# Optimization experiments

Measured on AMD Instinct MI355X. Metric: run time of the kernel, lower is better.

The kernel has to match this reference:

```python
import jax, jax.numpy as jnp
import numpy as np

LN_EPS = 1e-6

def _ln_proj(x, ln_scale, ln_bias, kernel, bias):
    # LayerNorm over last dim, then GEMM projection. Dropout is identity
    # (deterministic / eval mode, training=False default).
    mu = jnp.mean(x, axis=-1, keepdims=True)
    var = jnp.mean(jnp.square(x - mu), axis=-1, keepdims=True)
    xn = (x - mu) * jax.lax.rsqrt(var + LN_EPS) * ln_scale + ln_bias
    return jnp.einsum('bsh,hp->bsp', xn, kernel) + bias


def setup_inputs() -> dict:
    key = jax.random.key(0)
    ks = jax.random.split(key, 4)
    B, S, H, P = 2, 4096, 4096, 1024
    return {
        'vision_features': jax.random.normal(ks[0], (B, S, H), dtype=jnp.float32),
        'text_features': jax.random.normal(ks[1], (B, S, H), dtype=jnp.float32),
        'v_ln_scale': jnp.ones((H,), jnp.float32),
        'v_ln_bias': jnp.zeros((H,), jnp.float32),
        'v_kernel': jax.random.normal(ks[2], (H, P), dtype=jnp.float32) / np.sqrt(H).astype(np.float32),
        'v_bias': jnp.zeros((P,), jnp.float32),
        't_ln_scale': jnp.ones((H,), jnp.float32),
        't_ln_bias': jnp.zeros((H,), jnp.float32),
        't_kernel': jax.random.normal(ks[3], (H, P), dtype=jnp.float32) / np.sqrt(H).astype(np.float32),
        't_bias': jnp.zeros((P,), jnp.float32),
    }


def reference(vision_features, text_features, v_ln_scale, v_ln_bias, v_kernel, v_bias,
              t_ln_scale, t_ln_bias, t_kernel, t_bias):
    vision_projected = _ln_proj(vision_features, v_ln_scale, v_ln_bias, v_kernel, v_bias)
    text_projected = _ln_proj(text_features, t_ln_scale, t_ln_bias, t_kernel, t_bias)
    return (vision_projected, text_projected)
```

## Files before the change

kernel.cpp:

```cpp
#include <hip/hip_runtime.h>
#include <hip/hip_bf16.h>
#include <stdint.h>

#define LN_EPS 1e-6f

typedef __bf16 bf16x8 __attribute__((ext_vector_type(8)));
typedef float f32x4 __attribute__((ext_vector_type(4)));

__device__ __forceinline__ unsigned short f2bf(float f) {
    uint32_t u = __float_as_uint(f);
    uint32_t r = (u + 0x7fffu + ((u >> 16) & 1u)) >> 16;
    return (unsigned short)r;
}

__device__ __forceinline__ void async_copy16(const void* g, void* l) {
    const __attribute__((address_space(1))) uint32_t* gp =
        (const __attribute__((address_space(1))) uint32_t*)(uintptr_t)g;
    __attribute__((address_space(3))) uint32_t* lp =
        (__attribute__((address_space(3))) uint32_t*)(uint32_t)(uintptr_t)l;
    __builtin_amdgcn_global_load_lds(gp, lp, 16, 0, 0);
}

__global__ __launch_bounds__(256) void ln_bf16_kernel(
    const float* __restrict__ x0, const float* __restrict__ x1,
    const float* __restrict__ s0, const float* __restrict__ b0,
    const float* __restrict__ s1, const float* __restrict__ b1,
    unsigned short* __restrict__ y0, unsigned short* __restrict__ y1, int H)
{
    int wave = threadIdx.x >> 6, lane = threadIdx.x & 63;
    int row = blockIdx.x * 4 + wave;
    int prob = blockIdx.y;
    const float* x = (prob ? x1 : x0) + (size_t)row * H;
    const float* s = prob ? s1 : s0;
    const float* b = prob ? b1 : b0;
    unsigned short* y = (prob ? y1 : y0) + (size_t)row * H;

    float4 v[16];
    float sum = 0.f, sq = 0.f;
#pragma unroll
    for (int g = 0; g < 16; ++g) {
        v[g] = ((const float4*)x)[lane + 64 * g];
        sum += v[g].x + v[g].y + v[g].z + v[g].w;
        sq  += v[g].x * v[g].x + v[g].y * v[g].y + v[g].z * v[g].z + v[g].w * v[g].w;
    }
#pragma unroll
    for (int off = 32; off > 0; off >>= 1) {
        sum += __shfl_xor(sum, off, 64);
        sq  += __shfl_xor(sq, off, 64);
    }
    float mu = sum * (1.0f / 4096.0f);
    float var = sq * (1.0f / 4096.0f) - mu * mu;
    float rstd = rsqrtf(var + LN_EPS);

#pragma unroll
    for (int g = 0; g < 16; ++g) {
        int i4 = lane + 64 * g;
        float4 sc = ((const float4*)s)[i4];
        float4 bi = ((const float4*)b)[i4];
        ushort4 o;
        o.x = f2bf((v[g].x - mu) * rstd * sc.x + bi.x);
        o.y = f2bf((v[g].y - mu) * rstd * sc.y + bi.y);
        o.z = f2bf((v[g].z - mu) * rstd * sc.z + bi.z);
        o.w = f2bf((v[g].w - mu) * rstd * sc.w + bi.w);
        ((ushort4*)y)[i4] = o;
    }
}

__global__ __launch_bounds__(256) void cast_transpose_kernel(
    const float* __restrict__ w0, const float* __restrict__ w1,
    unsigned short* __restrict__ o0, unsigned short* __restrict__ o1,
    int K, int N)
{
    int prob = blockIdx.z;
    const float* w = prob ? w1 : w0;
    unsigned short* o = prob ? o1 : o0;
    __shared__ unsigned short tile[32][33];
    int tx = threadIdx.x & 31;
    int ty = threadIdx.x >> 5;
    int n0 = blockIdx.x * 32;
    int k0 = blockIdx.y * 32;
#pragma unroll
    for (int i = 0; i < 4; ++i) {
        int k = ty + 8 * i;
        tile[k][tx] = f2bf(w[(size_t)(k0 + k) * N + n0 + tx]);
    }
    __syncthreads();
#pragma unroll
    for (int i = 0; i < 4; ++i) {
        int n = ty + 8 * i;
        o[(size_t)(n0 + n) * K + k0 + tx] = tile[tx][n];
    }
}

#define BM 128
#define BN 128
#define BK 64

__global__ __launch_bounds__(256) void gemm_bf16_kernel(
    const unsigned short* __restrict__ A0, const unsigned short* __restrict__ A1,
    const unsigned short* __restrict__ W0, const unsigned short* __restrict__ W1,
    const float* __restrict__ bias0, const float* __restrict__ bias1,
    float* __restrict__ out0, float* __restrict__ out1,
    int M, int N, int K)
{
    int id = blockIdx.x;
    int xcd = id & 7;
    int l = id >> 3;
    int prob = l >> 6;
    int rem = l & 63;
    int mt = xcd * 8 + (rem >> 3);
    int nt = rem & 7;

    const unsigned short* A = prob ? A1 : A0;
    const unsigned short* W = prob ? W1 : W0;
    const float* bias = prob ? bias1 : bias0;
    float* out = prob ? out1 : out0;

    __shared__ unsigned short As[BM * BK];
    __shared__ unsigned short Bs[BN * BK];

    int t = threadIdx.x;
    int wave = t >> 6, lane = t & 63;
    int quad = lane >> 4, r16 = lane & 15;
    int wm = wave >> 1, wn = wave & 1;
    int kx = r16 & 7;

    int tile_m = mt * BM;
    int tile_n = nt * BN;

    const unsigned short* ga[4];
    const unsigned short* gb[4];
#pragma unroll
    for (int q = 0; q < 4; ++q) {
        int cc = q * 256 + t;
        int row = cc >> 3, kb = cc & 7;
        int kbg = kb ^ (row & 7);
        ga[q] = A + (size_t)(tile_m + row) * K + kbg * 8;
        gb[q] = W + (size_t)(tile_n + row) * K + kbg * 8;
    }

    f32x4 acc[4][4] = {};

    for (int k0 = 0; k0 < K; k0 += BK) {
#pragma unroll
        for (int q = 0; q < 4; ++q) {
            uint32_t lbase = (uint32_t)(q * 256 + wave * 64) * 16;
            async_copy16(ga[q] + k0, (char*)As + lbase);
            async_copy16(gb[q] + k0, (char*)Bs + lbase);
        }
        __syncthreads();

#pragma unroll
        for (int s = 0; s < 2; ++s) {
            bf16x8 af[4], bfr[4];
#pragma unroll
            for (int i = 0; i < 4; ++i) {
                int ka = (s * 4 + quad) ^ kx;
                af[i]  = *(const bf16x8*)(As + (wm * 64 + i * 16 + r16) * 64 + ka * 8);
                bfr[i] = *(const bf16x8*)(Bs + (wn * 64 + i * 16 + r16) * 64 + ka * 8);
            }
#pragma unroll
            for (int i = 0; i < 4; ++i)
#pragma unroll
                for (int j = 0; j < 4; ++j)
                    acc[i][j] = __builtin_amdgcn_mfma_f32_16x16x32_bf16(af[i], bfr[j], acc[i][j], 0, 0, 0);
        }
        __syncthreads();
    }

#pragma unroll
    for (int j = 0; j < 4; ++j) {
        int col = tile_n + wn * 64 + j * 16 + r16;
        float bj = bias[col];
#pragma unroll
        for (int i = 0; i < 4; ++i) {
            int row = tile_m + wm * 64 + i * 16 + quad * 4;
#pragma unroll
            for (int r = 0; r < 4; ++r)
                out[(size_t)(row + r) * N + col] = acc[i][j][r] + bj;
        }
    }
}

extern "C" void kernel_launch(void* const* d_in, const int* in_sizes, int n_in,
                              void* d_out, int out_size, void* d_ws, size_t ws_size,
                              hipStream_t stream) {
    const float* xv = (const float*)d_in[0];
    const float* xt = (const float*)d_in[1];
    const float* sv = (const float*)d_in[2];
    const float* bv = (const float*)d_in[3];
    const float* wv = (const float*)d_in[4];
    const float* biasv = (const float*)d_in[5];
    const float* st = (const float*)d_in[6];
    const float* bt = (const float*)d_in[7];
    const float* wt = (const float*)d_in[8];
    const float* biast = (const float*)d_in[9];
    float* out = (float*)d_out;

    const int B = 2, S = 4096, H = 4096, P = 1024;
    const int M = B * S;
    float* outv = out;
    float* outt = out + (size_t)M * P;

    size_t xnBytes = (size_t)M * H * 2;
    size_t wtBytes = (size_t)P * H * 2;
    char* ws = (char*)d_ws;

    if (ws_size >= 2 * xnBytes + 2 * wtBytes) {
        unsigned short* Xv = (unsigned short*)(ws);
        unsigned short* Xt = (unsigned short*)(ws + xnBytes);
        unsigned short* Wv = (unsigned short*)(ws + 2 * xnBytes);
        unsigned short* Wt = (unsigned short*)(ws + 2 * xnBytes + wtBytes);
        ln_bf16_kernel<<<dim3(M / 4, 2), 256, 0, stream>>>(xv, xt, sv, bv, st, bt, Xv, Xt, H);
        cast_transpose_kernel<<<dim3(P / 32, H / 32, 2), 256, 0, stream>>>(wv, wt, Wv, Wt, H, P);
        gemm_bf16_kernel<<<dim3(1024), 256, 0, stream>>>(
            Xv, Xt, Wv, Wt, biasv, biast, outv, outt, M, P, H);
    } else {
        unsigned short* X  = (unsigned short*)(ws);
        unsigned short* Wb = (unsigned short*)(ws + xnBytes);
        ln_bf16_kernel<<<dim3(M / 4, 1), 256, 0, stream>>>(xv, xv, sv, bv, sv, bv, X, X, H);
        cast_transpose_kernel<<<dim3(P / 32, H / 32, 1), 256, 0, stream>>>(wv, wv, Wb, Wb, H, P);
        gemm_bf16_kernel<<<dim3(512), 256, 0, stream>>>(
            X, X, Wb, Wb, biasv, biasv, outv, outv, M, P, H);
        ln_bf16_kernel<<<dim3(M / 4, 1), 256, 0, stream>>>(xt, xt, st, bt, st, bt, X, X, H);
        cast_transpose_kernel<<<dim3(P / 32, H / 32, 1), 256, 0, stream>>>(wt, wt, Wb, Wb, H, P);
        gemm_bf16_kernel<<<dim3(512), 256, 0, stream>>>(
            X, X, Wb, Wb, biast, biast, outt, outt, M, P, H);
    }
}
```

Measured before the change: 536.4 us.

## Double-buffer LDS tiles in bf16 GEMM to overlap loads with MFMA

The GEMM's A and B shared-memory tiles become two ping-pong buffers. A prologue loads the first K-tile, and each iteration issues async global-to-LDS copies for the next tile before running MFMAs on the current one. This removes one barrier per K step and aims to hide global load latency behind compute. In exchange, LDS use per block doubles to 64KB, which may lower the number of resident blocks per CU.

New measurement: 499.0 us. 1.07x faster.

```diff
diff --git a/kernel.cpp b/kernel.cpp
--- a/kernel.cpp
+++ b/kernel.cpp
@@ -116,8 +116,8 @@
     const float* bias = prob ? bias1 : bias0;
     float* out = prob ? out1 : out0;
 
-    __shared__ unsigned short As[BM * BK];
-    __shared__ unsigned short Bs[BN * BK];
+    __shared__ unsigned short As[2 * BM * BK];
+    __shared__ unsigned short Bs[2 * BM * BK];
 
     int t = threadIdx.x;
     int wave = t >> 6, lane = t & 63;
@@ -130,6 +130,7 @@
 
     const unsigned short* ga[4];
     const unsigned short* gb[4];
+    uint32_t lb[4];
 #pragma unroll
     for (int q = 0; q < 4; ++q) {
         int cc = q * 256 + t;
@@ -137,18 +138,34 @@
         int kbg = kb ^ (row & 7);
         ga[q] = A + (size_t)(tile_m + row) * K + kbg * 8;
         gb[q] = W + (size_t)(tile_n + row) * K + kbg * 8;
+        lb[q] = (uint32_t)(q * 256 + wave * 64) * 16;
     }
 
     f32x4 acc[4][4] = {};
 
-    for (int k0 = 0; k0 < K; k0 += BK) {
-#pragma unroll
-        for (int q = 0; q < 4; ++q) {
-            uint32_t lbase = (uint32_t)(q * 256 + wave * 64) * 16;
-            async_copy16(ga[q] + k0, (char*)As + lbase);
-            async_copy16(gb[q] + k0, (char*)Bs + lbase);
+#pragma unroll
+    for (int q = 0; q < 4; ++q) {
+        async_copy16(ga[q], (char*)As + lb[q]);
+        async_copy16(gb[q], (char*)Bs + lb[q]);
+    }
+    __syncthreads();
+
+    const int NTILES = K >> 6;
+    for (int kt = 0; kt < NTILES; ++kt) {
+        const int cur = kt & 1;
+        const unsigned short* cA = As + cur * (BM * BK);
+        const unsigned short* cB = Bs + cur * (BM * BK);
+
+        if (kt + 1 < NTILES) {
+            const int ko = (kt + 1) << 6;
+            char* dA = (char*)As + (cur ^ 1) * (BM * BK * 2);
+            char* dB = (char*)Bs + (cur ^ 1) * (BM * BK * 2);
+#pragma unroll
+            for (int q = 0; q < 4; ++q) {
+                async_copy16(ga[q] + ko, dA + lb[q]);
+                async_copy16(gb[q] + ko, dB + lb[q]);
+            }
         }
-        __syncthreads();
 
 #pragma unroll
         for (int s = 0; s < 2; ++s) {
@@ -156,8 +173,8 @@
 #pragma unroll
             for (int i = 0; i < 4; ++i) {
                 int ka = (s * 4 + quad) ^ kx;
-                af[i]  = *(const bf16x8*)(As + (wm * 64 + i * 16 + r16) * 64 + ka * 8);
-                bfr[i] = *(const bf16x8*)(Bs + (wn * 64 + i * 16 + r16) * 64 + ka * 8);
+                af[i]  = *(const bf16x8*)(cA + (wm * 64 + i * 16 + r16) * 64 + ka * 8);
+                bfr[i] = *(const bf16x8*)(cB + (wn * 64 + i * 16 + r16) * 64 + ka * 8);
             }
 #pragma unroll
             for (int i = 0; i < 4; ++i)
@@ -165,6 +182,7 @@
                 for (int j = 0; j < 4; ++j)
                     acc[i][j] = __builtin_amdgcn_mfma_f32_16x16x32_bf16(af[i], bfr[j], acc[i][j], 0, 0, 0);
         }
+
         __syncthreads();
     }
 
```

## Triple-buffer GEMM LDS tiles with async prefetch and vectorized epilogue

Applied to the files above, without the earlier changes.

Restructures the bf16 GEMM main loop into a three-stage LDS ring buffer with BK=32. Global-to-LDS async copies for future K tiles are issued while MFMAs run on the current tile, synchronised with explicit vmcnt waits and barriers. It also swaps the MFMA operand order so each lane holds contiguous output columns, which allows float4 stores with vector bias loads. Other additions are s_setprio around the MFMA block and a launch bound of 3 blocks per SM. The aim is to hide global load latency that the old load-then-sync loop exposed, at the cost of more barriers per K step and tighter register limits.

Result: faster. 506.4 us (-5.6%).

```diff
diff --git a/kernel.cpp b/kernel.cpp
--- a/kernel.cpp
+++ b/kernel.cpp
@@ -74,7 +74,7 @@
     int prob = blockIdx.z;
     const float* w = prob ? w1 : w0;
     unsigned short* o = prob ? o1 : o0;
-    __shared__ unsigned short tile[32][33];
+    __shared__ __align__(16) unsigned short tile[32][33];
     int tx = threadIdx.x & 31;
     int ty = threadIdx.x >> 5;
     int n0 = blockIdx.x * 32;
@@ -92,11 +92,47 @@
     }
 }
 
-#define BM 128
-#define BN 128
-#define BK 64
-
-__global__ __launch_bounds__(256) void gemm_bf16_kernel(
+#define BMg 128
+#define BNg 128
+#define BKg 32
+
+#define GEMM_TILE_ITER(VMSTR, PF)                                              \
+    {                                                                          \
+        const int bi = kt - (kt / 3) * 3;                                      \
+        const unsigned short* cA = As + bi * (BMg * BKg);                      \
+        const unsigned short* cB = Bs + bi * (BNg * BKg);                      \
+        asm volatile("s_waitcnt " VMSTR ::: "memory");                         \
+        __builtin_amdgcn_s_barrier();                                          \
+        __builtin_amdgcn_sched_barrier(0);                                     \
+        bf16x8 bfr[4], af[4];                                                  \
+        _Pragma("unroll")                                                      \
+        for (int j = 0; j < 4; ++j)                                            \
+            bfr[j] = *(const bf16x8*)(cB + (wn * 64 + j * 16 + r16) * 32 + ka * 8); \
+        _Pragma("unroll")                                                      \
+        for (int i = 0; i < 4; ++i)                                            \
+            af[i] = *(const bf16x8*)(cA + (wm * 64 + i * 16 + r16) * 32 + ka * 8);  \
+        __builtin_amdgcn_s_setprio(1);                                         \
+        _Pragma("unroll")                                                      \
+        for (int i = 0; i < 4; ++i)                                            \
+            _Pragma("unroll")                                                  \
+            for (int j = 0; j < 4; ++j)                                        \
+                acc[i][j] = __builtin_amdgcn_mfma_f32_16x16x32_bf16(           \
+                    bfr[j], af[i], acc[i][j], 0, 0, 0);                        \
+        __builtin_amdgcn_s_setprio(0);                                         \
+        __builtin_amdgcn_sched_barrier(0);                                     \
+        __builtin_amdgcn_s_barrier();                                          \
+        if (PF) {                                                              \
+            const int ko = (kt + 3) << 5;                                      \
+            char* dA = (char*)As + bi * (BMg * BKg * 2);                       \
+            char* dB = (char*)Bs + bi * (BNg * BKg * 2);                       \
+            _Pragma("unroll")                                                  \
+            for (int q = 0; q < 2; ++q) async_copy16(ga[q] + ko, dA + lba[q]); \
+            _Pragma("unroll")                                                  \
+            for (int q = 0; q < 2; ++q) async_copy16(gb[q] + ko, dB + lbb[q]); \
+        }                                                                      \
+    }
+
+__global__ __launch_bounds__(256, 3) void gemm_bf16_kernel(
     const unsigned short* __restrict__ A0, const unsigned short* __restrict__ A1,
     const unsigned short* __restrict__ W0, const unsigned short* __restrict__ W1,
     const float* __restrict__ bias0, const float* __restrict__ bias1,
@@ -116,68 +152,61 @@
     const float* bias = prob ? bias1 : bias0;
     float* out = prob ? out1 : out0;
 
-    __shared__ unsigned short As[BM * BK];
-    __shared__ unsigned short Bs[BN * BK];
+    __shared__ __align__(16) unsigned short As[3 * BMg * BKg];
+    __shared__ __align__(16) unsigned short Bs[3 * BNg * BKg];
 
     int t = threadIdx.x;
     int wave = t >> 6, lane = t & 63;
     int quad = lane >> 4, r16 = lane & 15;
     int wm = wave >> 1, wn = wave & 1;
-    int kx = r16 & 7;
-
-    int tile_m = mt * BM;
-    int tile_n = nt * BN;
-
-    const unsigned short* ga[4];
-    const unsigned short* gb[4];
-#pragma unroll
-    for (int q = 0; q < 4; ++q) {
+    int kx = (r16 >> 1) & 3;
+    int ka = quad ^ kx;
+
+    int tile_m = mt * BMg;
+    int tile_n = nt * BNg;
+
+    const unsigned short* ga[2];
+    const unsigned short* gb[2];
+    uint32_t lba[2], lbb[2];
+#pragma unroll
+    for (int q = 0; q < 2; ++q) {
         int cc = q * 256 + t;
-        int row = cc >> 3, kb = cc & 7;
-        int kbg = kb ^ (row & 7);
+        int row = cc >> 2, kb = cc & 3;
+        int kbg = kb ^ ((row >> 1) & 3);
         ga[q] = A + (size_t)(tile_m + row) * K + kbg * 8;
         gb[q] = W + (size_t)(tile_n + row) * K + kbg * 8;
+        lba[q] = lbb[q] = (uint32_t)(q * 256 + wave * 64) * 16;
     }
 
     f32x4 acc[4][4] = {};
 
-    for (int k0 = 0; k0 < K; k0 += BK) {
-#pragma unroll
-        for (int q = 0; q < 4; ++q) {
-            uint32_t lbase = (uint32_t)(q * 256 + wave * 64) * 16;
-            async_copy16(ga[q] + k0, (char*)As + lbase);
-            async_copy16(gb[q] + k0, (char*)Bs + lbase);
-        }
-        __syncthreads();
-
-#pragma unroll
-        for (int s = 0; s < 2; ++s) {
-            bf16x8 af[4], bfr[4];
-#pragma unroll
-            for (int i = 0; i < 4; ++i) {
-                int ka = (s * 4 + quad) ^ kx;
-                af[i]  = *(const bf16x8*)(As + (wm * 64 + i * 16 + r16) * 64 + ka * 8);
-                bfr[i] = *(const bf16x8*)(Bs + (wn * 64 + i * 16 + r16) * 64 + ka * 8);
-            }
-#pragma unroll
-            for (int i = 0; i < 4; ++i)
-#pragma unroll
-                for (int j = 0; j < 4; ++j)
-                    acc[i][j] = __builtin_amdgcn_mfma_f32_16x16x32_bf16(af[i], bfr[j], acc[i][j], 0, 0, 0);
-        }
-        __syncthreads();
-    }
-
-#pragma unroll
-    for (int j = 0; j < 4; ++j) {
-        int col = tile_n + wn * 64 + j * 16 + r16;
-        float bj = bias[col];
-#pragma unroll
-        for (int i = 0; i < 4; ++i) {
-            int row = tile_m + wm * 64 + i * 16 + quad * 4;
-#pragma unroll
-            for (int r = 0; r < 4; ++r)
-                out[(size_t)(row + r) * N + col] = acc[i][j][r] + bj;
+#pragma unroll
+    for (int tt = 0; tt < 3; ++tt) {
+        const int ko = tt << 5;
+        char* dA = (char*)As + tt * (BMg * BKg * 2);
+        char* dB = (char*)Bs + tt * (BNg * BKg * 2);
+#pragma unroll
+        for (int q = 0; q < 2; ++q) async_copy16(ga[q] + ko, dA + lba[q]);
+#pragma unroll
+        for (int q = 0; q < 2; ++q) async_copy16(gb[q] + ko, dB + lbb[q]);
+    }
+
+    const int NT = K >> 5;
+    int kt = 0;
+    for (; kt <= NT - 3; ++kt) GEMM_TILE_ITER("vmcnt(8)", (kt + 3 < NT))
+    GEMM_TILE_ITER("vmcnt(4)", false)
+    ++kt;
+    GEMM_TILE_ITER("vmcnt(0)", false)
+
+#pragma unroll
+    for (int i = 0; i < 4; ++i) {
+        size_t row = (size_t)(tile_m + wm * 64 + i * 16 + r16);
+        float* orow = out + row * N;
+#pragma unroll
+        for (int j = 0; j < 4; ++j) {
+            int ncol = tile_n + wn * 64 + j * 16 + quad * 4;
+            f32x4 v = acc[i][j] + *(const f32x4*)(bias + ncol);
+            *(f32x4*)(orow + ncol) = v;
         }
     }
 }
```
